# Performance work log

Measured on AMD Instinct MI355X. Metric: run time of the kernel, lower is better.

Reference implementation:

```python
import jax, jax.numpy as jnp
import numpy as np

NUM_USERS = 1000000
NUM_ITEMS = 500000
NUM_R = 5
D = 64
B = 512
N = 30


def _mlp3(x, W1, b1, W2, b2, W3, b3):
    # Linear->ReLU->Linear->ReLU->Linear (as in MLP module)
    h = jax.nn.relu(x @ W1 + b1)
    h = jax.nn.relu(h @ W2 + b2)
    return h @ W3 + b3


def _attn(self_rep, neighs, W1, b1, W2, b2):
    # pi_rep = self_rep.unsqueeze(1).expand_as(neighs)
    rep = jnp.broadcast_to(jnp.expand_dims(self_rep, 1), neighs.shape)
    h = jax.nn.relu(jnp.concatenate([rep, neighs], -1) @ W1 + b1)
    s = h @ W2 + b2
    # NOTE: original torch code uses F.softmax(..., dim=0) (over the batch axis); kept faithfully
    return jax.nn.softmax(s, axis=0)


def _forward(fl, nodes_u, nodes_i, u_items_list, u_users_list, i_users_list,
             u_items_r, u_users_items, u_users_items_r, i_users_r):
    (E_u, E_i, E_r,
     gv_W1, gv_b1, gv_W2, gv_b2, gv_W3, gv_b3,
     attI_W1, attI_b1, attI_W2, attI_b2,
     attO_W1, attO_b1, attO_W2, attO_b2,
     attS_W1, attS_b1, attS_W2, attS_b2,
     atti_W1, atti_b1, atti_W2, atti_b2,
     linI_W, linI_b, linO_W, linO_b,
     umlp_W1, umlp_b1, umlp_W2, umlp_b2, umlp_W3, umlp_b3,
     gu_W1, gu_b1, gu_W2, gu_b2, gu_W3, gu_b3,
     ilin_W, ilin_b,
     g_W1, g_b1, g_W2, g_b2, g_W3, g_b3) = fl

    # ----- UserModeling: item-space aggregation -----
    pi = E_u[nodes_u]                                   # [B, d]
    er = E_r[u_items_r]                                 # [B, N, d]
    qa = E_i[u_items_list]                              # [B, N, d]
    xia = _mlp3(jnp.concatenate([qa, er], -1), gv_W1, gv_b1, gv_W2, gv_b2, gv_W3, gv_b3)
    alpha_ia = _attn(pi, xia, attI_W1, attI_b1, attI_W2, attI_b2)   # [B, N, 1]
    hi_I = jax.nn.relu(jnp.sum(alpha_ia * xia, 1) @ linI_W + linI_b)  # [B, d]

    # ----- UserModeling: social-space aggregation -----
    po = E_u[u_users_list]                              # [B, N, d]
    ero = E_r[u_users_items_r]                          # [B, N, N, d]
    qao = E_i[u_users_items]                            # [B, N, N, d]
    xoa = _mlp3(jnp.concatenate([qao, ero], -1), gv_W1, gv_b1, gv_W2, gv_b2, gv_W3, gv_b3)
    alpha_oa = _attn(po, xoa, attO_W1, attO_b1, attO_W2, attO_b2)   # [B, N, N, 1]
    ho_I = jax.nn.relu(jnp.sum(alpha_oa * xoa, 1) @ linO_W + linO_b)  # [B, N, d]
    # original att_S(ho_I, pi) does not shape-check; intended semantics: pi is self, ho_I are neighbors
    beta_io = _attn(pi, ho_I, attS_W1, attS_b1, attS_W2, attS_b2)   # [B, N, 1]
    hi_S = jax.nn.relu(jnp.sum(beta_io * ho_I, 1) @ linO_W + linO_b)  # original reuses linO (linS unused)
    hi = _mlp3(jnp.concatenate([hi_I, hi_S], -1), umlp_W1, umlp_b1, umlp_W2, umlp_b2, umlp_W3, umlp_b3)

    # ----- ItemModeling -----
    qj = E_i[nodes_i]                                   # [B, d]
    pt = E_u[i_users_list]                              # [B, N, d]
    er2 = E_r[i_users_r]                                # [B, N, d]
    fjt = _mlp3(jnp.concatenate([pt, er2], -1), gu_W1, gu_b1, gu_W2, gu_b2, gu_W3, gu_b3)
    mu_jt = _attn(qj, fjt, atti_W1, atti_b1, atti_W2, atti_b2)      # [B, N, 1]
    zj = jax.nn.relu(jnp.sum(mu_jt * fjt, 1) @ ilin_W + ilin_b)     # [B, d]

    # ----- Rating prediction -----
    gl = _mlp3(jnp.concatenate([hi, zj], -1), g_W1, g_b1, g_W2, g_b2, g_W3, g_b3)  # [B, 1]
    return gl


def setup_inputs() -> dict:
    key = jax.random.key(0)
    ks = iter(jax.random.split(key, 80))
    def P(*shape):
        return jax.random.normal(next(ks), shape, jnp.float32) * 0.05
    def I(shape, hi):
        return jax.random.randint(next(ks), shape, 0, hi, dtype=jnp.int32)
    d = D
    inp = {}
    inp['E_u'] = P(NUM_USERS, d)
    inp['E_i'] = P(NUM_ITEMS, d)
    inp['E_r'] = P(NUM_R, d)
    for pre in ['gv', 'umlp', 'gu']:
        inp[pre + '_W1'] = P(2 * d, d); inp[pre + '_b1'] = P(d)
        inp[pre + '_W2'] = P(d, d);     inp[pre + '_b2'] = P(d)
        inp[pre + '_W3'] = P(d, d);     inp[pre + '_b3'] = P(d)
    for pre in ['attI', 'attO', 'attS', 'atti']:
        inp[pre + '_W1'] = P(2 * d, d); inp[pre + '_b1'] = P(d)
        inp[pre + '_W2'] = P(d, 1);     inp[pre + '_b2'] = P(1)
    inp['linI_W'] = P(d, d); inp['linI_b'] = P(d)
    inp['linO_W'] = P(d, d); inp['linO_b'] = P(d)
    inp['ilin_W'] = P(d, d); inp['ilin_b'] = P(d)
    inp['g_W1'] = P(2 * d, 1); inp['g_b1'] = P(1)
    inp['g_W2'] = P(1, 1);     inp['g_b2'] = P(1)
    inp['g_W3'] = P(1, 1);     inp['g_b3'] = P(1)
    inp['nodes_u'] = I((B,), NUM_USERS)
    inp['nodes_i'] = I((B,), NUM_ITEMS)
    inp['u_items_list'] = I((B, N), NUM_ITEMS)
    inp['u_users_list'] = I((B, N), NUM_USERS)
    inp['i_users_list'] = I((B, N), NUM_USERS)
    inp['u_items_r'] = I((B, N), NUM_R)
    inp['u_users_items'] = I((B, N, N), NUM_ITEMS)
    inp['u_users_items_r'] = I((B, N, N), NUM_R)
    inp['i_users_r'] = I((B, N), NUM_R)
    return inp


def reference(E_u, E_i, E_r,
              gv_W1, gv_b1, gv_W2, gv_b2, gv_W3, gv_b3,
              attI_W1, attI_b1, attI_W2, attI_b2,
              attO_W1, attO_b1, attO_W2, attO_b2,
              attS_W1, attS_b1, attS_W2, attS_b2,
              atti_W1, atti_b1, atti_W2, atti_b2,
              linI_W, linI_b, linO_W, linO_b,
              umlp_W1, umlp_b1, umlp_W2, umlp_b2, umlp_W3, umlp_b3,
              gu_W1, gu_b1, gu_W2, gu_b2, gu_W3, gu_b3,
              ilin_W, ilin_b,
              g_W1, g_b1, g_W2, g_b2, g_W3, g_b3,
              nodes_u, nodes_i, u_items_list, u_users_list, i_users_list,
              u_items_r, u_users_items, u_users_items_r, i_users_r):
    fl = (E_u, E_i, E_r,
          gv_W1, gv_b1, gv_W2, gv_b2, gv_W3, gv_b3,
          attI_W1, attI_b1, attI_W2, attI_b2,
          attO_W1, attO_b1, attO_W2, attO_b2,
          attS_W1, attS_b1, attS_W2, attS_b2,
          atti_W1, atti_b1, atti_W2, atti_b2,
          linI_W, linI_b, linO_W, linO_b,
          umlp_W1, umlp_b1, umlp_W2, umlp_b2, umlp_W3, umlp_b3,
          gu_W1, gu_b1, gu_W2, gu_b2, gu_W3, gu_b3,
          ilin_W, ilin_b,
          g_W1, g_b1, g_W2, g_b2, g_W3, g_b3)
    return _forward(fl, nodes_u, nodes_i, u_items_list, u_users_list, i_users_list,
                    u_items_r, u_users_items, u_users_items_r, i_users_r)
```

## Files before the change

### kernel.cpp

```cpp
#include <hip/hip_runtime.h>
#include <cstdint>
#include <cstddef>


#define GB 512
#define GN 30
#define GD 64

typedef unsigned short u16;
typedef __attribute__((ext_vector_type(8))) short short8v;
typedef __attribute__((ext_vector_type(4))) float f32x4;

__device__ __forceinline__ u16 f2bf(float x) {
  union { float f; uint32_t u; } c; c.f = x;
  uint32_t r = c.u + 0x7fffu + ((c.u >> 16) & 1u);
  return (u16)(r >> 16);
}
__device__ __forceinline__ float bf2f(u16 b) {
  union { float f; uint32_t u; } c; c.u = ((uint32_t)b) << 16; return c.f;
}
__device__ __forceinline__ float wave_sum(float v) {
#pragma unroll
  for (int off = 32; off >= 1; off >>= 1) v += __shfl_xor(v, off, 64);
  return v;
}


__device__ __forceinline__ void mfma_3layers(
    int lane, int wave,
    const u16* xs, const u16* w1s, const u16* w2s, const u16* w3s,
    const float* b1s, const float* b2s, u16* hs, f32x4* c3) {
  const int m = lane & 15, quad = lane >> 4;
  const int row = wave * 16 + m;
  const f32x4 zz = {0.f, 0.f, 0.f, 0.f};
  f32x4 cc[4];
#pragma unroll
  for (int c = 0; c < 4; c++) cc[c] = zz;
#pragma unroll
  for (int kk = 0; kk < 4; kk++) {
    short8v av = *(const short8v*)(xs + row * 136 + kk * 32 + quad * 8);
#pragma unroll
    for (int c = 0; c < 4; c++) {
      short8v bv = *(const short8v*)(w1s + (c * 16 + m) * 136 + kk * 32 + quad * 8);
      cc[c] = __builtin_amdgcn_mfma_f32_16x16x32_bf16(av, bv, cc[c], 0, 0, 0);
    }
  }
#pragma unroll
  for (int c = 0; c < 4; c++)
#pragma unroll
    for (int r = 0; r < 4; r++) {
      int rr = wave * 16 + quad * 4 + r;
      hs[rr * 72 + c * 16 + m] = f2bf(fmaxf(cc[c][r] + b1s[c * 16 + m], 0.f));
    }
#pragma unroll
  for (int c = 0; c < 4; c++) cc[c] = zz;
#pragma unroll
  for (int kk = 0; kk < 2; kk++) {
    short8v av = *(const short8v*)(hs + row * 72 + kk * 32 + quad * 8);
#pragma unroll
    for (int c = 0; c < 4; c++) {
      short8v bv = *(const short8v*)(w2s + (c * 16 + m) * 72 + kk * 32 + quad * 8);
      cc[c] = __builtin_amdgcn_mfma_f32_16x16x32_bf16(av, bv, cc[c], 0, 0, 0);
    }
  }
#pragma unroll
  for (int c = 0; c < 4; c++)
#pragma unroll
    for (int r = 0; r < 4; r++) {
      int rr = wave * 16 + quad * 4 + r;
      hs[rr * 72 + c * 16 + m] = f2bf(fmaxf(cc[c][r] + b2s[c * 16 + m], 0.f));
    }
#pragma unroll
  for (int c = 0; c < 4; c++) c3[c] = zz;
#pragma unroll
  for (int kk = 0; kk < 2; kk++) {
    short8v av = *(const short8v*)(hs + row * 72 + kk * 32 + quad * 8);
#pragma unroll
    for (int c = 0; c < 4; c++) {
      short8v bv = *(const short8v*)(w3s + (c * 16 + m) * 72 + kk * 32 + quad * 8);
      c3[c] = __builtin_amdgcn_mfma_f32_16x16x32_bf16(av, bv, c3[c], 0, 0, 0);
    }
  }
}

__global__ void k_prep(const float* __restrict__ gvW1, const float* __restrict__ gvW2,
                       const float* __restrict__ gvW3, const float* __restrict__ aOW1,
                       const float* __restrict__ guW1, const float* __restrict__ guW2,
                       const float* __restrict__ guW3,
                       u16* gv1t, u16* gv2t, u16* gv3t, u16* aot,
                       u16* gu1t, u16* gu2t, u16* gu3t) {
  int i = blockIdx.x * 256 + threadIdx.x;
  const float* src; u16* dst; int sh; int o = i;
  if (o < 8192)        { src = gvW1;           dst = gv1t; sh = 7; }
  else if (o < 12288)  { o -= 8192;  src = gvW2; dst = gv2t; sh = 6; }
  else if (o < 16384)  { o -= 12288; src = gvW3; dst = gv3t; sh = 6; }
  else if (o < 20480)  { o -= 16384; src = aOW1 + 64 * 64; dst = aot; sh = 6; }
  else if (o < 28672)  { o -= 20480; src = guW1; dst = gu1t; sh = 7; }
  else if (o < 32768)  { o -= 28672; src = guW2; dst = gu2t; sh = 6; }
  else                 { o -= 32768; src = guW3; dst = gu3t; sh = 6; }
  int n = o >> sh, k = o & ((1 << sh) - 1);
  dst[(size_t)n * (1 << sh) + k] = f2bf(src[(size_t)k * 64 + n]);
}

__global__ __launch_bounds__(256, 2) void k_mlp3_mfma(
    const float* __restrict__ tabA, const int* __restrict__ idxA,
    const float* __restrict__ tabB, const int* __restrict__ idxB,
    const u16* __restrict__ w1t, const u16* __restrict__ w2t, const u16* __restrict__ w3t,
    const float* __restrict__ b1, const float* __restrict__ b2, const float* __restrict__ b3,
    float* __restrict__ out) {
  __shared__ __align__(16) u16 xs[64 * 136], w1s[64 * 136], w2s[64 * 72], w3s[64 * 72], hs[64 * 72];
  __shared__ float b1s[64], b2s[64], b3s[64];
  int t = threadIdx.x;
  for (int i = t; i < 64 * 16; i += 256) { int n = i >> 4, j = i & 15;
    ((uint4*)(w1s + n * 136))[j] = ((const uint4*)(w1t + n * 128))[j]; }
  for (int i = t; i < 64 * 8; i += 256) { int n = i >> 3, j = i & 7;
    ((uint4*)(w2s + n * 72))[j] = ((const uint4*)(w2t + n * 64))[j];
    ((uint4*)(w3s + n * 72))[j] = ((const uint4*)(w3t + n * 64))[j]; }
  if (t < 64) { b1s[t] = b1[t]; b2s[t] = b2[t]; b3s[t] = b3[t]; }
  int base = blockIdx.x * 64;
  { int lr = t >> 2, q = t & 3; int row = base + lr;
    const float* src = (q < 2) ? (tabA + (size_t)idxA[row] * 64 + q * 32)
                               : (tabB + (size_t)idxB[row] * 64 + (q - 2) * 32);
    u16* dst = xs + lr * 136 + q * 32;
    const float4* s4 = (const float4*)src;
#pragma unroll
    for (int h = 0; h < 8; h++) { float4 v = s4[h]; ushort4 u;
      u.x = f2bf(v.x); u.y = f2bf(v.y); u.z = f2bf(v.z); u.w = f2bf(v.w);
      *(ushort4*)(dst + h * 4) = u; }
  }
  __syncthreads();
  int lane = t & 63, wave = t >> 6;
  f32x4 c3[4];
  mfma_3layers(lane, wave, xs, w1s, w2s, w3s, b1s, b2s, hs, c3);
  int m = lane & 15, quad = lane >> 4;
#pragma unroll
  for (int c = 0; c < 4; c++)
#pragma unroll
    for (int r = 0; r < 4; r++) {
      int rr = wave * 16 + quad * 4 + r;
      out[(size_t)(base + rr) * 64 + c * 16 + m] = c3[c][r] + b3s[c * 16 + m];
    }
}

__global__ __launch_bounds__(256, 2) void k_xoa1_mfma(
    const float* __restrict__ E_i, const float* __restrict__ E_r,
    const int* __restrict__ items, const int* __restrict__ items_r,
    const u16* __restrict__ w1t, const u16* __restrict__ w2t, const u16* __restrict__ w3t,
    const float* __restrict__ b1, const float* __restrict__ b2, const float* __restrict__ b3,
    const u16* __restrict__ aot, const float* __restrict__ ab1,
    const float* __restrict__ aW2, const float* __restrict__ ab2,
    const float* __restrict__ poW, u16* __restrict__ xoa_bf,
    float* __restrict__ sOut) {
  __shared__ __align__(16) u16 xs[64 * 136], w1s[64 * 136], w2s[64 * 72], w3s[64 * 72], was[64 * 72], hs[64 * 72];
  __shared__ float b1s[64], b2s[64], b3s[64], ab1s[64], aw2s[64];
  int t = threadIdx.x;
  for (int i = t; i < 64 * 16; i += 256) { int n = i >> 4, j = i & 15;
    ((uint4*)(w1s + n * 136))[j] = ((const uint4*)(w1t + n * 128))[j]; }
  for (int i = t; i < 64 * 8; i += 256) { int n = i >> 3, j = i & 7;
    ((uint4*)(w2s + n * 72))[j] = ((const uint4*)(w2t + n * 64))[j];
    ((uint4*)(w3s + n * 72))[j] = ((const uint4*)(w3t + n * 64))[j];
    ((uint4*)(was + n * 72))[j] = ((const uint4*)(aot + n * 64))[j]; }
  if (t < 64) { b1s[t] = b1[t]; b2s[t] = b2[t]; b3s[t] = b3[t];
                ab1s[t] = ab1[t]; aw2s[t] = aW2[t]; }
  __syncthreads();
  const int lane = t & 63, wave = t >> 6;
  const int m = lane & 15, quad = lane >> 4;
  const int lr = t >> 2, q = t & 3;
  const float ab2v = ab2[0];
  const f32x4 zz = {0.f, 0.f, 0.f, 0.f};
  for (int tile = blockIdx.x; tile < (GB * GN * GN) / 64; tile += gridDim.x) {
    int base = tile * 64;
    { int row = base + lr;
      const float* src = (q < 2) ? (E_i + (size_t)items[row] * 64 + q * 32)
                                 : (E_r + (size_t)items_r[row] * 64 + (q - 2) * 32);
      u16* dst = xs + lr * 136 + q * 32;
      const float4* s4 = (const float4*)src;
#pragma unroll
      for (int h = 0; h < 8; h++) { float4 v = s4[h]; ushort4 u;
        u.x = f2bf(v.x); u.y = f2bf(v.y); u.z = f2bf(v.z); u.w = f2bf(v.w);
        *(ushort4*)(dst + h * 4) = u; }
    }
    f32x4 c3[4];
    mfma_3layers(lane, wave, xs, w1s, w2s, w3s, b1s, b2s, hs, c3);
#pragma unroll
    for (int c = 0; c < 4; c++)
#pragma unroll
      for (int r = 0; r < 4; r++) {
        int rr = wave * 16 + quad * 4 + r;
        hs[rr * 72 + c * 16 + m] = f2bf(c3[c][r] + b3s[c * 16 + m]);
      }
#pragma unroll
    for (int c2 = 0; c2 < 2; c2++) {
      int chunk = lane * 2 + c2;
      int row = chunk >> 3, k = chunk & 7;
      *(uint4*)(xoa_bf + ((size_t)(base + wave * 16 + row)) * 64 + k * 8) =
          *(const uint4*)(hs + (wave * 16 + row) * 72 + k * 8);
    }
    f32x4 c4[4];
#pragma unroll
    for (int c = 0; c < 4; c++) c4[c] = zz;
    int row = wave * 16 + m;
#pragma unroll
    for (int kk = 0; kk < 2; kk++) {
      short8v av = *(const short8v*)(hs + row * 72 + kk * 32 + quad * 8);
#pragma unroll
      for (int c = 0; c < 4; c++) {
        short8v bv = *(const short8v*)(was + (c * 16 + m) * 72 + kk * 32 + quad * 8);
        c4[c] = __builtin_amdgcn_mfma_f32_16x16x32_bf16(av, bv, c4[c], 0, 0, 0);
      }
    }
    float part[4] = {0.f, 0.f, 0.f, 0.f};
#pragma unroll
    for (int r = 0; r < 4; r++) {
      int gRow = base + wave * 16 + quad * 4 + r;
      int b_ = gRow / (GN * GN);
      int n2 = gRow % GN;
      const float* pw = poW + ((size_t)b_ * GN + n2) * 64;
#pragma unroll
      for (int c = 0; c < 4; c++) {
        int col = c * 16 + m;
        float h = c4[c][r] + pw[col] + ab1s[col];
        part[r] += fmaxf(h, 0.f) * aw2s[col];
      }
    }
#pragma unroll
    for (int r = 0; r < 4; r++) {
      float v = part[r];
      v += __shfl_xor(v, 1, 64); v += __shfl_xor(v, 2, 64);
      v += __shfl_xor(v, 4, 64); v += __shfl_xor(v, 8, 64);
      if (m == 0) sOut[base + wave * 16 + quad * 4 + r] = v + ab2v;
    }
  }
}

__global__ __launch_bounds__(256) void k_ho(
    const u16* __restrict__ xoa_bf, const float* __restrict__ alpha,
    const float* __restrict__ linW, const float* __restrict__ linB,
    float* __restrict__ ho) {
  __shared__ float lws[64 * 64];
  __shared__ float lbs[64];
  __shared__ float ts[4][64];
  int t = threadIdx.x;
  for (int i = t; i < 4096; i += 256) lws[i] = linW[i];
  if (t < 64) lbs[t] = linB[t];
  __syncthreads();
  int lane = t & 63, wave = t >> 6;
  int gid = blockIdx.x * 4 + wave;
  int b_ = gid / GN, n2 = gid - b_ * GN;
  float acc = 0.f;
  for (int n1 = 0; n1 < GN; n1++) {
    size_t row = (size_t)(b_ * GN + n1) * GN + n2;
    float al = alpha[row];
    acc = fmaf(al, bf2f(xoa_bf[row * 64 + lane]), acc);
  }
  ts[wave][lane] = acc;
  float o = lbs[lane];
#pragma unroll 8
  for (int k = 0; k < 64; k++) o = fmaf(ts[wave][k], lws[k * 64 + lane], o);
  ho[(size_t)gid * 64 + lane] = fmaxf(o, 0.f);
}

template <int R>
__device__ __forceinline__ void mlp3_rows(
    int lane, const float* const* pa, const float* const* pb,
    const u16* w1s, const u16* w2s, const u16* w3s,
    const float* b1s, const float* b2s, const float* b3s,
    float (*hbw)[GD], float* acc) {
#pragma unroll
  for (int r = 0; r < R; r++) acc[r] = b1s[lane];
#pragma unroll 8
  for (int k = 0; k < 64; k++) {
    float w = bf2f(w1s[k * 64 + lane]);
#pragma unroll
    for (int r = 0; r < R; r++) acc[r] = fmaf(pa[r][k], w, acc[r]);
  }
#pragma unroll 8
  for (int k = 0; k < 64; k++) {
    float w = bf2f(w1s[(64 + k) * 64 + lane]);
#pragma unroll
    for (int r = 0; r < R; r++) acc[r] = fmaf(pb[r][k], w, acc[r]);
  }
#pragma unroll
  for (int r = 0; r < R; r++) hbw[r][lane] = fmaxf(acc[r], 0.f);
#pragma unroll
  for (int r = 0; r < R; r++) acc[r] = b2s[lane];
#pragma unroll
  for (int kc = 0; kc < 16; kc++) {
    float w0 = bf2f(w2s[(kc * 4 + 0) * 64 + lane]);
    float w1 = bf2f(w2s[(kc * 4 + 1) * 64 + lane]);
    float w2 = bf2f(w2s[(kc * 4 + 2) * 64 + lane]);
    float w3 = bf2f(w2s[(kc * 4 + 3) * 64 + lane]);
#pragma unroll
    for (int r = 0; r < R; r++) {
      float4 x = *(const float4*)(&hbw[r][kc * 4]);
      acc[r] = fmaf(x.x, w0, fmaf(x.y, w1, fmaf(x.z, w2, fmaf(x.w, w3, acc[r]))));
    }
  }
#pragma unroll
  for (int r = 0; r < R; r++) hbw[r][lane] = fmaxf(acc[r], 0.f);
#pragma unroll
  for (int r = 0; r < R; r++) acc[r] = b3s[lane];
#pragma unroll
  for (int kc = 0; kc < 16; kc++) {
    float w0 = bf2f(w3s[(kc * 4 + 0) * 64 + lane]);
    float w1 = bf2f(w3s[(kc * 4 + 1) * 64 + lane]);
    float w2 = bf2f(w3s[(kc * 4 + 2) * 64 + lane]);
    float w3 = bf2f(w3s[(kc * 4 + 3) * 64 + lane]);
#pragma unroll
    for (int r = 0; r < R; r++) {
      float4 x = *(const float4*)(&hbw[r][kc * 4]);
      acc[r] = fmaf(x.x, w0, fmaf(x.y, w1, fmaf(x.z, w2, fmaf(x.w, w3, acc[r]))));
    }
  }
}

__global__ __launch_bounds__(256, 4) void k_rowlin(
    int M, const float* __restrict__ tab, const int* __restrict__ idx,
    const float* __restrict__ W, float* __restrict__ out) {
  __shared__ float ws[64 * 64];
  for (int i = threadIdx.x; i < 64 * 64; i += 256) ws[i] = W[i];
  __syncthreads();
  const int lane = threadIdx.x & 63, wave = threadIdx.x >> 6;
  int base0 = (blockIdx.x * 4 + wave) * 8;
  if (base0 >= M) return;
  const float* p[8];
#pragma unroll
  for (int r = 0; r < 8; r++) {
    int ia = __builtin_amdgcn_readfirstlane(idx[base0 + r]);
    p[r] = tab + (size_t)ia * 64;
  }
  float acc[8];
#pragma unroll
  for (int r = 0; r < 8; r++) acc[r] = 0.f;
#pragma unroll 8
  for (int k = 0; k < 64; k++) {
    float w = ws[k * 64 + lane];
#pragma unroll
    for (int r = 0; r < 8; r++) acc[r] = fmaf(p[r][k], w, acc[r]);
  }
#pragma unroll
  for (int r = 0; r < 8; r++) out[(size_t)(base0 + r) * 64 + lane] = acc[r];
}

__global__ __launch_bounds__(512, 2) void k_mlp3(
    int M,
    const float* __restrict__ tabA, const int* __restrict__ idxA,
    const float* __restrict__ tabB, const int* __restrict__ idxB,
    const float* __restrict__ W1, const float* __restrict__ b1,
    const float* __restrict__ W2, const float* __restrict__ b2,
    const float* __restrict__ W3, const float* __restrict__ b3,
    float* __restrict__ out) {
  __shared__ u16 w1s[128 * 64], w2s[64 * 64], w3s[64 * 64];
  __shared__ float b1s[64], b2s[64], b3s[64];
  __shared__ float hb[8][8][GD];
  for (int i = threadIdx.x; i < 128 * 64; i += 512) w1s[i] = f2bf(W1[i]);
  for (int i = threadIdx.x; i < 64 * 64; i += 512) { w2s[i] = f2bf(W2[i]); w3s[i] = f2bf(W3[i]); }
  if (threadIdx.x < 64) { b1s[threadIdx.x] = b1[threadIdx.x]; b2s[threadIdx.x] = b2[threadIdx.x]; b3s[threadIdx.x] = b3[threadIdx.x]; }
  __syncthreads();
  const int lane = threadIdx.x & 63, wave = threadIdx.x >> 6;
  for (int base = blockIdx.x * 64; base < M; base += gridDim.x * 64) {
    int rb = base + wave * 8;
    const float* pa[8]; const float* pb[8];
#pragma unroll
    for (int r = 0; r < 8; r++) {
      int row = rb + r;
      int ia = idxA ? idxA[row] : row;
      pa[r] = tabA + (size_t)__builtin_amdgcn_readfirstlane(ia) * 64;
      int ib = idxB ? idxB[row] : row;
      pb[r] = tabB + (size_t)__builtin_amdgcn_readfirstlane(ib) * 64;
    }
    float acc[8];
    mlp3_rows<8>(lane, pa, pb, w1s, w2s, w3s, b1s, b2s, b3s, hb[wave], acc);
#pragma unroll
    for (int r = 0; r < 8; r++) out[(size_t)(rb + r) * 64 + lane] = acc[r];
  }
}

__global__ __launch_bounds__(256, 4) void k_score(
    int M, const float* __restrict__ selfW, const float* __restrict__ X,
    const float* __restrict__ W1b, const float* __restrict__ b1,
    const float* __restrict__ W2, const float* __restrict__ b2,
    float* __restrict__ sOut) {
  __shared__ float ws[64 * 64];
  __shared__ float w2s[64], b1s[64];
  for (int i = threadIdx.x; i < 64 * 64; i += 256) ws[i] = W1b[i];
  if (threadIdx.x < 64) { w2s[threadIdx.x] = W2[threadIdx.x]; b1s[threadIdx.x] = b1[threadIdx.x]; }
  __syncthreads();
  const int lane = threadIdx.x & 63, wave = threadIdx.x >> 6;
  int rb = (blockIdx.x * 4 + wave) * 8;
  if (rb >= M) return;
  const float* px[8]; float acc[8];
#pragma unroll
  for (int r = 0; r < 8; r++) {
    int row = rb + r;
    px[r] = X + (size_t)row * 64;
    acc[r] = b1s[lane] + selfW[(size_t)(row / GN) * 64 + lane];
  }
#pragma unroll 8
  for (int k = 0; k < 64; k++) {
    float w = ws[k * 64 + lane];
#pragma unroll
    for (int r = 0; r < 8; r++) acc[r] = fmaf(px[r][k], w, acc[r]);
  }
  float bb2 = b2[0];
#pragma unroll
  for (int r = 0; r < 8; r++) {
    float v = fmaxf(acc[r], 0.f) * w2s[lane];
    v = wave_sum(v);
    if (lane == 0) sOut[rb + r] = v + bb2;
  }
}

__global__ __launch_bounds__(256) void k_softmax_col(float* __restrict__ s, int C) {
  int c = blockIdx.x, t = threadIdx.x;
  int lane = t & 63, wave = t >> 6;
  float v0 = s[(size_t)t * C + c];
  float v1 = s[(size_t)(t + 256) * C + c];
  float m = fmaxf(v0, v1);
#pragma unroll
  for (int off = 32; off >= 1; off >>= 1) m = fmaxf(m, __shfl_xor(m, off, 64));
  __shared__ float rm[4], rs[4];
  if (lane == 0) rm[wave] = m;
  __syncthreads();
  float M4 = fmaxf(fmaxf(rm[0], rm[1]), fmaxf(rm[2], rm[3]));
  float e0 = expf(v0 - M4), e1 = expf(v1 - M4);
  float sm = wave_sum(e0 + e1);
  if (lane == 0) rs[wave] = sm;
  __syncthreads();
  float inv = 1.f / (rs[0] + rs[1] + rs[2] + rs[3]);
  s[(size_t)t * C + c] = e0 * inv;
  s[(size_t)(t + 256) * C + c] = e1 * inv;
}

__global__ __launch_bounds__(64) void k_wsum_lin(
    int C, const float* __restrict__ alpha, const float* __restrict__ X,
    const float* __restrict__ W, const float* __restrict__ bias,
    float* __restrict__ out) {
  int b = blockIdx.x, l = threadIdx.x;
  float t = 0.f;
  for (int n = 0; n < C; n++) t = fmaf(alpha[b * C + n], X[((size_t)b * C + n) * 64 + l], t);
  __shared__ float ts[64];
  ts[l] = t;
  float acc = bias[l];
#pragma unroll 8
  for (int k = 0; k < 64; k++) acc = fmaf(ts[k], W[k * 64 + l], acc);
  out[(size_t)b * 64 + l] = fmaxf(acc, 0.f);
}

__global__ __launch_bounds__(256) void k_final(
    const float* __restrict__ hi, const float* __restrict__ zj,
    const float* __restrict__ gW1, const float* __restrict__ gb1,
    const float* __restrict__ gW2, const float* __restrict__ gb2,
    const float* __restrict__ gW3, const float* __restrict__ gb3,
    float* __restrict__ out) {
  const int lane = threadIdx.x & 63, wave = threadIdx.x >> 6;
  int b = blockIdx.x * 4 + wave;
  float v = hi[(size_t)b * 64 + lane] * gW1[lane] + zj[(size_t)b * 64 + lane] * gW1[64 + lane];
  v = wave_sum(v);
  if (lane == 0) {
    float h = fmaxf(v + gb1[0], 0.f);
    h = fmaxf(h * gW2[0] + gb2[0], 0.f);
    out[b] = h * gW3[0] + gb3[0];
  }
}

extern "C" void kernel_launch(void* const* d_in, const int* in_sizes, int n_in,
                              void* d_out, int out_size, void* d_ws, size_t ws_size,
                              hipStream_t stream) {
  const float* E_u = (const float*)d_in[0];
  const float* E_i = (const float*)d_in[1];
  const float* E_r = (const float*)d_in[2];
  const float* gvW1 = (const float*)d_in[3];  const float* gvb1 = (const float*)d_in[4];
  const float* gvW2 = (const float*)d_in[5];  const float* gvb2 = (const float*)d_in[6];
  const float* gvW3 = (const float*)d_in[7];  const float* gvb3 = (const float*)d_in[8];
  const float* umW1 = (const float*)d_in[9];  const float* umb1 = (const float*)d_in[10];
  const float* umW2 = (const float*)d_in[11]; const float* umb2 = (const float*)d_in[12];
  const float* umW3 = (const float*)d_in[13]; const float* umb3 = (const float*)d_in[14];
  const float* guW1 = (const float*)d_in[15]; const float* gub1 = (const float*)d_in[16];
  const float* guW2 = (const float*)d_in[17]; const float* gub2 = (const float*)d_in[18];
  const float* guW3 = (const float*)d_in[19]; const float* gub3 = (const float*)d_in[20];
  const float* aIW1 = (const float*)d_in[21]; const float* aIb1 = (const float*)d_in[22];
  const float* aIW2 = (const float*)d_in[23]; const float* aIb2 = (const float*)d_in[24];
  const float* aOW1 = (const float*)d_in[25]; const float* aOb1 = (const float*)d_in[26];
  const float* aOW2 = (const float*)d_in[27]; const float* aOb2 = (const float*)d_in[28];
  const float* aSW1 = (const float*)d_in[29]; const float* aSb1 = (const float*)d_in[30];
  const float* aSW2 = (const float*)d_in[31]; const float* aSb2 = (const float*)d_in[32];
  const float* aiW1 = (const float*)d_in[33]; const float* aib1 = (const float*)d_in[34];
  const float* aiW2 = (const float*)d_in[35]; const float* aib2 = (const float*)d_in[36];
  const float* linIW = (const float*)d_in[37]; const float* linIb = (const float*)d_in[38];
  const float* linOW = (const float*)d_in[39]; const float* linOb = (const float*)d_in[40];
  const float* ilinW = (const float*)d_in[41]; const float* ilinb = (const float*)d_in[42];
  const float* gW1 = (const float*)d_in[43]; const float* gb1 = (const float*)d_in[44];
  const float* gW2 = (const float*)d_in[45]; const float* gb2 = (const float*)d_in[46];
  const float* gW3 = (const float*)d_in[47]; const float* gb3 = (const float*)d_in[48];
  const int* nodes_u = (const int*)d_in[49];
  const int* nodes_i = (const int*)d_in[50];
  const int* u_items = (const int*)d_in[51];
  const int* u_users = (const int*)d_in[52];
  const int* i_users = (const int*)d_in[53];
  const int* u_items_r = (const int*)d_in[54];
  const int* uu_items = (const int*)d_in[55];
  const int* uu_items_r = (const int*)d_in[56];
  const int* i_users_r = (const int*)d_in[57];
  float* out = (float*)d_out;

  float* p = (float*)d_ws;
  float* piWI = p; p += GB * GD;
  float* piWS = p; p += GB * GD;
  float* qjWi = p; p += GB * GD;
  float* poW  = p; p += GB * GN * GD;
  float* xia  = p; p += GB * GN * GD;
  float* fjt  = p; p += GB * GN * GD;
  float* ho   = p; p += GB * GN * GD;
  float* sI   = p; p += GB * GN;
  float* sS   = p; p += GB * GN;
  float* si   = p; p += GB * GN;
  float* sO   = p; p += GB * GN * GN;
  float* hiI  = p; p += GB * GD;
  float* hiS  = p; p += GB * GD;
  float* hi   = p; p += GB * GD;
  float* zj   = p; p += GB * GD;
  u16* q16 = (u16*)p;
  u16* gv1t = q16; q16 += 8192;
  u16* gv2t = q16; q16 += 4096;
  u16* gv3t = q16; q16 += 4096;
  u16* aot  = q16; q16 += 4096;
  u16* gu1t = q16; q16 += 8192;
  u16* gu2t = q16; q16 += 4096;
  u16* gu3t = q16; q16 += 4096;
  u16* xoa_bf = q16; q16 += (size_t)GB * GN * GN * GD;

  const int BN = GB * GN;
  const int M2 = GB * GN * GN;

  k_prep<<<144, 256, 0, stream>>>(gvW1, gvW2, gvW3, aOW1, guW1, guW2, guW3,
                                  gv1t, gv2t, gv3t, aot, gu1t, gu2t, gu3t);
  k_rowlin<<<GB / 32, 256, 0, stream>>>(GB, E_u, nodes_u, aIW1, piWI);
  k_rowlin<<<GB / 32, 256, 0, stream>>>(GB, E_u, nodes_u, aSW1, piWS);
  k_rowlin<<<GB / 32, 256, 0, stream>>>(GB, E_i, nodes_i, aiW1, qjWi);
  k_rowlin<<<BN / 32, 256, 0, stream>>>(BN, E_u, u_users, aOW1, poW);

  k_mlp3_mfma<<<BN / 64, 256, 0, stream>>>(E_i, u_items, E_r, u_items_r,
                                           gv1t, gv2t, gv3t, gvb1, gvb2, gvb3, xia);
  k_score<<<BN / 32, 256, 0, stream>>>(BN, piWI, xia, aIW1 + 64 * 64, aIb1, aIW2, aIb2, sI);
  k_softmax_col<<<GN, 256, 0, stream>>>(sI, GN);
  k_wsum_lin<<<GB, 64, 0, stream>>>(GN, sI, xia, linIW, linIb, hiI);

  k_xoa1_mfma<<<512, 256, 0, stream>>>(E_i, E_r, uu_items, uu_items_r,
                                       gv1t, gv2t, gv3t, gvb1, gvb2, gvb3,
                                       aot, aOb1, aOW2, aOb2, poW, xoa_bf, sO);
  k_softmax_col<<<GN * GN, 256, 0, stream>>>(sO, GN * GN);
  k_ho<<<BN / 4, 256, 0, stream>>>(xoa_bf, sO, linOW, linOb, ho);
  k_score<<<BN / 32, 256, 0, stream>>>(BN, piWS, ho, aSW1 + 64 * 64, aSb1, aSW2, aSb2, sS);
  k_softmax_col<<<GN, 256, 0, stream>>>(sS, GN);
  k_wsum_lin<<<GB, 64, 0, stream>>>(GN, sS, ho, linOW, linOb, hiS);
  k_mlp3<<<GB / 64, 512, 0, stream>>>(GB, hiI, nullptr, hiS, nullptr,
                                      umW1, umb1, umW2, umb2, umW3, umb3, hi);

  k_mlp3_mfma<<<BN / 64, 256, 0, stream>>>(E_u, i_users, E_r, i_users_r,
                                           gu1t, gu2t, gu3t, gub1, gub2, gub3, fjt);
  k_score<<<BN / 32, 256, 0, stream>>>(BN, qjWi, fjt, aiW1 + 64 * 64, aib1, aiW2, aib2, si);
  k_softmax_col<<<GN, 256, 0, stream>>>(si, GN);
  k_wsum_lin<<<GB, 64, 0, stream>>>(GN, si, fjt, ilinW, ilinb, zj);

  k_final<<<GB / 4, 256, 0, stream>>>(hi, zj, gW1, gb1, gW2, gb2, gW3, gb3, out);
}
```

Baseline: 722.4 us.

## Merge pipeline into setup, fused MLP-attention engine, aggregation and tail kernels

Replaces about twenty launches with roughly eight. Weight prep and the row projections are merged into one setup kernel. All three MLP+attention-score paths (xoa, xia, fjt) run in one persistent engine kernel that keeps the layer-2, layer-3 and attention weights in registers and prefetches the next tile's gathered rows. The intermediates xia and fjt are now stored as bf16, scores are stored transposed for softmax, and the user MLP plus the final MLP are fused into one MFMA tail kernel. The aim is to cut launch overhead, shared-memory weight traffic and global intermediate bandwidth, at the cost of higher register pressure and some extra bf16 precision loss.

After: 616.5 us. -14.7%, faster.

```diff
diff --git a/kernel.cpp b/kernel.cpp
--- a/kernel.cpp
+++ b/kernel.cpp
@@ -6,6 +6,7 @@
 #define GB 512
 #define GN 30
 #define GD 64
+#define IDX16(l) ((((l) & 15) << 2) | ((l) >> 4))
 
 typedef unsigned short u16;
 typedef __attribute__((ext_vector_type(8))) short short8v;
@@ -25,362 +26,316 @@
   return v;
 }
 
-
-__device__ __forceinline__ void mfma_3layers(
-    int lane, int wave,
-    const u16* xs, const u16* w1s, const u16* w2s, const u16* w3s,
-    const float* b1s, const float* b2s, u16* hs, f32x4* c3) {
-  const int m = lane & 15, quad = lane >> 4;
-  const int row = wave * 16 + m;
-  const f32x4 zz = {0.f, 0.f, 0.f, 0.f};
-  f32x4 cc[4];
-#pragma unroll
-  for (int c = 0; c < 4; c++) cc[c] = zz;
-#pragma unroll
-  for (int kk = 0; kk < 4; kk++) {
-    short8v av = *(const short8v*)(xs + row * 136 + kk * 32 + quad * 8);
-#pragma unroll
-    for (int c = 0; c < 4; c++) {
-      short8v bv = *(const short8v*)(w1s + (c * 16 + m) * 136 + kk * 32 + quad * 8);
-      cc[c] = __builtin_amdgcn_mfma_f32_16x16x32_bf16(av, bv, cc[c], 0, 0, 0);
-    }
-  }
-#pragma unroll
-  for (int c = 0; c < 4; c++)
-#pragma unroll
-    for (int r = 0; r < 4; r++) {
-      int rr = wave * 16 + quad * 4 + r;
-      hs[rr * 72 + c * 16 + m] = f2bf(fmaxf(cc[c][r] + b1s[c * 16 + m], 0.f));
-    }
-#pragma unroll
-  for (int c = 0; c < 4; c++) cc[c] = zz;
-#pragma unroll
-  for (int kk = 0; kk < 2; kk++) {
-    short8v av = *(const short8v*)(hs + row * 72 + kk * 32 + quad * 8);
-#pragma unroll
-    for (int c = 0; c < 4; c++) {
-      short8v bv = *(const short8v*)(w2s + (c * 16 + m) * 72 + kk * 32 + quad * 8);
-      cc[c] = __builtin_amdgcn_mfma_f32_16x16x32_bf16(av, bv, cc[c], 0, 0, 0);
-    }
-  }
-#pragma unroll
-  for (int c = 0; c < 4; c++)
-#pragma unroll
-    for (int r = 0; r < 4; r++) {
-      int rr = wave * 16 + quad * 4 + r;
-      hs[rr * 72 + c * 16 + m] = f2bf(fmaxf(cc[c][r] + b2s[c * 16 + m], 0.f));
-    }
-#pragma unroll
-  for (int c = 0; c < 4; c++) c3[c] = zz;
-#pragma unroll
-  for (int kk = 0; kk < 2; kk++) {
-    short8v av = *(const short8v*)(hs + row * 72 + kk * 32 + quad * 8);
-#pragma unroll
-    for (int c = 0; c < 4; c++) {
-      short8v bv = *(const short8v*)(w3s + (c * 16 + m) * 72 + kk * 32 + quad * 8);
-      c3[c] = __builtin_amdgcn_mfma_f32_16x16x32_bf16(av, bv, c3[c], 0, 0, 0);
-    }
-  }
-}
-
-__global__ void k_prep(const float* __restrict__ gvW1, const float* __restrict__ gvW2,
-                       const float* __restrict__ gvW3, const float* __restrict__ aOW1,
-                       const float* __restrict__ guW1, const float* __restrict__ guW2,
-                       const float* __restrict__ guW3,
-                       u16* gv1t, u16* gv2t, u16* gv3t, u16* aot,
-                       u16* gu1t, u16* gu2t, u16* gu3t) {
-  int i = blockIdx.x * 256 + threadIdx.x;
-  const float* src; u16* dst; int sh; int o = i;
-  if (o < 8192)        { src = gvW1;           dst = gv1t; sh = 7; }
-  else if (o < 12288)  { o -= 8192;  src = gvW2; dst = gv2t; sh = 6; }
-  else if (o < 16384)  { o -= 12288; src = gvW3; dst = gv3t; sh = 6; }
-  else if (o < 20480)  { o -= 16384; src = aOW1 + 64 * 64; dst = aot; sh = 6; }
-  else if (o < 28672)  { o -= 20480; src = guW1; dst = gu1t; sh = 7; }
-  else if (o < 32768)  { o -= 28672; src = guW2; dst = gu2t; sh = 6; }
-  else                 { o -= 32768; src = guW3; dst = gu3t; sh = 6; }
-  int n = o >> sh, k = o & ((1 << sh) - 1);
-  dst[(size_t)n * (1 << sh) + k] = f2bf(src[(size_t)k * 64 + n]);
-}
-
-__global__ __launch_bounds__(256, 2) void k_mlp3_mfma(
-    const float* __restrict__ tabA, const int* __restrict__ idxA,
-    const float* __restrict__ tabB, const int* __restrict__ idxB,
-    const u16* __restrict__ w1t, const u16* __restrict__ w2t, const u16* __restrict__ w3t,
-    const float* __restrict__ b1, const float* __restrict__ b2, const float* __restrict__ b3,
-    float* __restrict__ out) {
-  __shared__ __align__(16) u16 xs[64 * 136], w1s[64 * 136], w2s[64 * 72], w3s[64 * 72], hs[64 * 72];
-  __shared__ float b1s[64], b2s[64], b3s[64];
-  int t = threadIdx.x;
+__global__ __launch_bounds__(256) void k_setup(
+    const float* __restrict__ gvW1, const float* __restrict__ gvW2, const float* __restrict__ gvW3,
+    const float* __restrict__ guW1, const float* __restrict__ guW2, const float* __restrict__ guW3,
+    const float* __restrict__ umW1, const float* __restrict__ umW2, const float* __restrict__ umW3,
+    const float* __restrict__ aOW1, const float* __restrict__ aIW1, const float* __restrict__ aiW1,
+    const float* __restrict__ aSW1,
+    const float* __restrict__ E_u, const float* __restrict__ E_i,
+    const int* __restrict__ nodes_u, const int* __restrict__ nodes_i, const int* __restrict__ u_users,
+    u16* gv1t, u16* gv2t, u16* gv3t, u16* gu1t, u16* gu2t, u16* gu3t,
+    u16* um1t, u16* um2t, u16* um3t, u16* aOt, u16* aIt, u16* ait,
+    float* piWI, float* piWS, float* qjWi, float* poW) {
+  __shared__ float ws[64 * 64];
+  int blk = blockIdx.x, t = threadIdx.x;
+  if (blk < 240) {
+    int o = blk * 256 + t;
+    const float* src; u16* dst; int kind;
+    if      (o < 8192)  {            src = gvW1; dst = gv1t; kind = 0; }
+    else if (o < 12288) { o -= 8192;  src = gvW2; dst = gv2t; kind = 1; }
+    else if (o < 16384) { o -= 12288; src = gvW3; dst = gv3t; kind = 1; }
+    else if (o < 20480) { o -= 16384; src = aOW1; dst = aOt;  kind = 2; }
+    else if (o < 28672) { o -= 20480; src = guW1; dst = gu1t; kind = 0; }
+    else if (o < 32768) { o -= 28672; src = guW2; dst = gu2t; kind = 1; }
+    else if (o < 36864) { o -= 32768; src = guW3; dst = gu3t; kind = 1; }
+    else if (o < 40960) { o -= 36864; src = aIW1; dst = aIt;  kind = 2; }
+    else if (o < 45056) { o -= 40960; src = aiW1; dst = ait;  kind = 2; }
+    else if (o < 53248) { o -= 45056; src = umW1; dst = um1t; kind = 0; }
+    else if (o < 57344) { o -= 53248; src = umW2; dst = um2t; kind = 1; }
+    else                { o -= 57344; src = umW3; dst = um3t; kind = 1; }
+    if (kind == 0) { int n = o >> 7, k = o & 127; dst[n * 128 + k] = f2bf(src[(size_t)k * 64 + n]); }
+    else { int n = o >> 6, p = o & 63; int k = ((p & 3) << 4) | (p >> 2); if (kind == 2) k += 64;
+           dst[n * 64 + p] = f2bf(src[(size_t)k * 64 + n]); }
+    return;
+  }
+  int rb = blk - 240;
+  const float* tab; const int* idx; const float* W; float* out; int base;
+  if (rb < 16)      { tab = E_u; idx = nodes_u; W = aIW1; out = piWI; base = rb * 32; }
+  else if (rb < 32) { tab = E_u; idx = nodes_u; W = aSW1; out = piWS; base = (rb - 16) * 32; }
+  else if (rb < 48) { tab = E_i; idx = nodes_i; W = aiW1; out = qjWi; base = (rb - 32) * 32; }
+  else              { tab = E_u; idx = u_users; W = aOW1; out = poW;  base = (rb - 48) * 32; }
+  for (int i = t; i < 4096; i += 256) ws[i] = W[i];
+  __syncthreads();
+  int lane = t & 63, wave = t >> 6;
+  int b0 = base + wave * 8;
+  const float* p[8]; float acc[8];
+#pragma unroll
+  for (int r = 0; r < 8; r++) {
+    p[r] = tab + (size_t)__builtin_amdgcn_readfirstlane(idx[b0 + r]) * 64;
+    acc[r] = 0.f;
+  }
+#pragma unroll 8
+  for (int k = 0; k < 64; k++) {
+    float w = ws[k * 64 + lane];
+#pragma unroll
+    for (int r = 0; r < 8; r++) acc[r] = fmaf(p[r][k], w, acc[r]);
+  }
+#pragma unroll
+  for (int r = 0; r < 8; r++) out[(size_t)(b0 + r) * 64 + lane] = acc[r];
+}
+
+__global__ __launch_bounds__(256, 2) void k_engine(
+    const float* __restrict__ E_i, const float* __restrict__ E_r, const float* __restrict__ E_u,
+    const int* __restrict__ uu_items, const int* __restrict__ uu_items_r,
+    const int* __restrict__ u_items, const int* __restrict__ u_items_r,
+    const int* __restrict__ i_users, const int* __restrict__ i_users_r,
+    const u16* __restrict__ gv1t, const u16* __restrict__ gv2t, const u16* __restrict__ gv3t,
+    const u16* __restrict__ gu1t, const u16* __restrict__ gu2t, const u16* __restrict__ gu3t,
+    const float* __restrict__ gvb1, const float* __restrict__ gvb2, const float* __restrict__ gvb3,
+    const float* __restrict__ gub1, const float* __restrict__ gub2, const float* __restrict__ gub3,
+    const u16* __restrict__ aOt, const u16* __restrict__ aIt, const u16* __restrict__ ait,
+    const float* __restrict__ aOb1, const float* __restrict__ aIb1, const float* __restrict__ aib1,
+    const float* __restrict__ aOW2, const float* __restrict__ aIW2, const float* __restrict__ aiW2,
+    const float* __restrict__ aOb2, const float* __restrict__ aIb2, const float* __restrict__ aib2,
+    const float* __restrict__ poW, const float* __restrict__ piWI, const float* __restrict__ qjWi,
+    u16* __restrict__ xoa_bf, u16* __restrict__ xia_bf, u16* __restrict__ fjt_bf,
+    float* __restrict__ sOT, float* __restrict__ sIT, float* __restrict__ siT) {
+  __shared__ __align__(16) u16 xs[64 * 136], w1s[64 * 136], hs[64 * 72];
+  __shared__ float b1s[64], b2s[64], b3s[64], ab1s[64], aw2s[64];
+  int t = threadIdx.x, blk = blockIdx.x;
+  const float *tabA, *tabB, *selfW, *b1, *b2, *b3, *ab1, *aW2, *ab2p;
+  const int *idxA, *idxB; const u16 *w1t, *w2t, *w3t, *att;
+  u16* outB; float* sT; int tile0, modeNN;
+  if (blk < 480) {
+    tabA = E_i; idxA = uu_items; tabB = E_r; idxB = uu_items_r;
+    w1t = gv1t; w2t = gv2t; w3t = gv3t; b1 = gvb1; b2 = gvb2; b3 = gvb3;
+    att = aOt; ab1 = aOb1; aW2 = aOW2; ab2p = aOb2; selfW = poW;
+    outB = xoa_bf; sT = sOT; tile0 = blk * 15; modeNN = 1;
+  } else if (blk < 496) {
+    int lb = blk - 480;
+    tabA = E_i; idxA = u_items; tabB = E_r; idxB = u_items_r;
+    w1t = gv1t; w2t = gv2t; w3t = gv3t; b1 = gvb1; b2 = gvb2; b3 = gvb3;
+    att = aIt; ab1 = aIb1; aW2 = aIW2; ab2p = aIb2; selfW = piWI;
+    outB = xia_bf; sT = sIT; tile0 = lb * 15; modeNN = 0;
+  } else {
+    int lb = blk - 496;
+    tabA = E_u; idxA = i_users; tabB = E_r; idxB = i_users_r;
+    w1t = gu1t; w2t = gu2t; w3t = gu3t; b1 = gub1; b2 = gub2; b3 = gub3;
+    att = ait; ab1 = aib1; aW2 = aiW2; ab2p = aib2; selfW = qjWi;
+    outB = fjt_bf; sT = siT; tile0 = lb * 15; modeNN = 0;
+  }
+  const int nt = 15;
   for (int i = t; i < 64 * 16; i += 256) { int n = i >> 4, j = i & 15;
     ((uint4*)(w1s + n * 136))[j] = ((const uint4*)(w1t + n * 128))[j]; }
-  for (int i = t; i < 64 * 8; i += 256) { int n = i >> 3, j = i & 7;
-    ((uint4*)(w2s + n * 72))[j] = ((const uint4*)(w2t + n * 64))[j];
-    ((uint4*)(w3s + n * 72))[j] = ((const uint4*)(w3t + n * 64))[j]; }
-  if (t < 64) { b1s[t] = b1[t]; b2s[t] = b2[t]; b3s[t] = b3[t]; }
-  int base = blockIdx.x * 64;
-  { int lr = t >> 2, q = t & 3; int row = base + lr;
+  if (t < 64) { b1s[t] = b1[t]; b2s[t] = b2[t]; b3s[t] = b3[t];
+                ab1s[t] = ab1[t]; aw2s[t] = aW2[t]; }
+  __syncthreads();
+  const int lane = t & 63, wave = t >> 6, m = lane & 15, quad = lane >> 4;
+  const int lr = t >> 2, q = t & 3;
+  short8v w2f[8], w3f[8], waf[8];
+#pragma unroll
+  for (int c = 0; c < 4; c++)
+#pragma unroll
+    for (int kk = 0; kk < 2; kk++) {
+      int off = (c * 16 + m) * 64 + kk * 32 + quad * 8;
+      w2f[c * 2 + kk] = *(const short8v*)(w2t + off);
+      w3f[c * 2 + kk] = *(const short8v*)(w3t + off);
+      waf[c * 2 + kk] = *(const short8v*)(att + off);
+    }
+  const float ab2v = ab2p[0];
+  const f32x4 zz = {0.f, 0.f, 0.f, 0.f};
+  float4 fr[8];
+  {
+    int row = tile0 * 64 + lr;
     const float* src = (q < 2) ? (tabA + (size_t)idxA[row] * 64 + q * 32)
                                : (tabB + (size_t)idxB[row] * 64 + (q - 2) * 32);
-    u16* dst = xs + lr * 136 + q * 32;
-    const float4* s4 = (const float4*)src;
-#pragma unroll
-    for (int h = 0; h < 8; h++) { float4 v = s4[h]; ushort4 u;
-      u.x = f2bf(v.x); u.y = f2bf(v.y); u.z = f2bf(v.z); u.w = f2bf(v.w);
-      *(ushort4*)(dst + h * 4) = u; }
-  }
-  __syncthreads();
-  int lane = t & 63, wave = t >> 6;
-  f32x4 c3[4];
-  mfma_3layers(lane, wave, xs, w1s, w2s, w3s, b1s, b2s, hs, c3);
-  int m = lane & 15, quad = lane >> 4;
-#pragma unroll
-  for (int c = 0; c < 4; c++)
-#pragma unroll
-    for (int r = 0; r < 4; r++) {
-      int rr = wave * 16 + quad * 4 + r;
-      out[(size_t)(base + rr) * 64 + c * 16 + m] = c3[c][r] + b3s[c * 16 + m];
-    }
-}
-
-__global__ __launch_bounds__(256, 2) void k_xoa1_mfma(
-    const float* __restrict__ E_i, const float* __restrict__ E_r,
-    const int* __restrict__ items, const int* __restrict__ items_r,
-    const u16* __restrict__ w1t, const u16* __restrict__ w2t, const u16* __restrict__ w3t,
-    const float* __restrict__ b1, const float* __restrict__ b2, const float* __restrict__ b3,
-    const u16* __restrict__ aot, const float* __restrict__ ab1,
-    const float* __restrict__ aW2, const float* __restrict__ ab2,
-    const float* __restrict__ poW, u16* __restrict__ xoa_bf,
-    float* __restrict__ sOut) {
-  __shared__ __align__(16) u16 xs[64 * 136], w1s[64 * 136], w2s[64 * 72], w3s[64 * 72], was[64 * 72], hs[64 * 72];
-  __shared__ float b1s[64], b2s[64], b3s[64], ab1s[64], aw2s[64];
-  int t = threadIdx.x;
-  for (int i = t; i < 64 * 16; i += 256) { int n = i >> 4, j = i & 15;
-    ((uint4*)(w1s + n * 136))[j] = ((const uint4*)(w1t + n * 128))[j]; }
-  for (int i = t; i < 64 * 8; i += 256) { int n = i >> 3, j = i & 7;
-    ((uint4*)(w2s + n * 72))[j] = ((const uint4*)(w2t + n * 64))[j];
-    ((uint4*)(w3s + n * 72))[j] = ((const uint4*)(w3t + n * 64))[j];
-    ((uint4*)(was + n * 72))[j] = ((const uint4*)(aot + n * 64))[j]; }
-  if (t < 64) { b1s[t] = b1[t]; b2s[t] = b2[t]; b3s[t] = b3[t];
-                ab1s[t] = ab1[t]; aw2s[t] = aW2[t]; }
-  __syncthreads();
-  const int lane = t & 63, wave = t >> 6;
-  const int m = lane & 15, quad = lane >> 4;
-  const int lr = t >> 2, q = t & 3;
-  const float ab2v = ab2[0];
-  const f32x4 zz = {0.f, 0.f, 0.f, 0.f};
-  for (int tile = blockIdx.x; tile < (GB * GN * GN) / 64; tile += gridDim.x) {
-    int base = tile * 64;
-    { int row = base + lr;
-      const float* src = (q < 2) ? (E_i + (size_t)items[row] * 64 + q * 32)
-                                 : (E_r + (size_t)items_r[row] * 64 + (q - 2) * 32);
-      u16* dst = xs + lr * 136 + q * 32;
-      const float4* s4 = (const float4*)src;
-#pragma unroll
-      for (int h = 0; h < 8; h++) { float4 v = s4[h]; ushort4 u;
+#pragma unroll
+    for (int h = 0; h < 8; h++) fr[h] = ((const float4*)src)[h];
+  }
+  for (int it = 0; it < nt; it++) {
+    int base = (tile0 + it) * 64;
+    { u16* dst = xs + lr * 136 + q * 32;
+#pragma unroll
+      for (int h = 0; h < 8; h++) { float4 v = fr[h]; ushort4 u;
         u.x = f2bf(v.x); u.y = f2bf(v.y); u.z = f2bf(v.z); u.w = f2bf(v.w);
-        *(ushort4*)(dst + h * 4) = u; }
-    }
+        *(ushort4*)(dst + h * 4) = u; } }
+    if (it + 1 < nt) {
+      int row = base + 64 + lr;
+      const float* src = (q < 2) ? (tabA + (size_t)idxA[row] * 64 + q * 32)
+                                 : (tabB + (size_t)idxB[row] * 64 + (q - 2) * 32);
+#pragma unroll
+      for (int h = 0; h < 8; h++) fr[h] = ((const float4*)src)[h];
+    }
+    f32x4 cc[4];
+#pragma unroll
+    for (int c = 0; c < 4; c++) cc[c] = zz;
+#pragma unroll
+    for (int kk = 0; kk < 4; kk++) {
+      short8v av = *(const short8v*)(xs + (wave * 16 + m) * 136 + kk * 32 + quad * 8);
+#pragma unroll
+      for (int c = 0; c < 4; c++) {
+        short8v bv = *(const short8v*)(w1s + (c * 16 + m) * 136 + kk * 32 + quad * 8);
+        cc[c] = __builtin_amdgcn_mfma_f32_16x16x32_bf16(av, bv, cc[c], 0, 0, 0);
+      }
+    }
+#pragma unroll
+    for (int r = 0; r < 4; r++) { ushort4 u;
+      u.x = f2bf(fmaxf(cc[0][r] + b1s[m], 0.f));
+      u.y = f2bf(fmaxf(cc[1][r] + b1s[16 + m], 0.f));
+      u.z = f2bf(fmaxf(cc[2][r] + b1s[32 + m], 0.f));
+      u.w = f2bf(fmaxf(cc[3][r] + b1s[48 + m], 0.f));
+      *(ushort4*)(hs + (wave * 16 + quad * 4 + r) * 72 + m * 4) = u; }
+#pragma unroll
+    for (int c = 0; c < 4; c++) cc[c] = zz;
+#pragma unroll
+    for (int kk = 0; kk < 2; kk++) {
+      short8v av = *(const short8v*)(hs + (wave * 16 + m) * 72 + kk * 32 + quad * 8);
+#pragma unroll
+      for (int c = 0; c < 4; c++)
+        cc[c] = __builtin_amdgcn_mfma_f32_16x16x32_bf16(av, w2f[c * 2 + kk], cc[c], 0, 0, 0);
+    }
+#pragma unroll
+    for (int r = 0; r < 4; r++) { ushort4 u;
+      u.x = f2bf(fmaxf(cc[0][r] + b2s[m], 0.f));
+      u.y = f2bf(fmaxf(cc[1][r] + b2s[16 + m], 0.f));
+      u.z = f2bf(fmaxf(cc[2][r] + b2s[32 + m], 0.f));
+      u.w = f2bf(fmaxf(cc[3][r] + b2s[48 + m], 0.f));
+      *(ushort4*)(hs + (wave * 16 + quad * 4 + r) * 72 + m * 4) = u; }
     f32x4 c3[4];
-    mfma_3layers(lane, wave, xs, w1s, w2s, w3s, b1s, b2s, hs, c3);
-#pragma unroll
-    for (int c = 0; c < 4; c++)
-#pragma unroll
-      for (int r = 0; r < 4; r++) {
-        int rr = wave * 16 + quad * 4 + r;
-        hs[rr * 72 + c * 16 + m] = f2bf(c3[c][r] + b3s[c * 16 + m]);
-      }
+#pragma unroll
+    for (int c = 0; c < 4; c++) c3[c] = zz;
+#pragma unroll
+    for (int kk = 0; kk < 2; kk++) {
+      short8v av = *(const short8v*)(hs + (wave * 16 + m) * 72 + kk * 32 + quad * 8);
+#pragma unroll
+      for (int c = 0; c < 4; c++)
+        c3[c] = __builtin_amdgcn_mfma_f32_16x16x32_bf16(av, w3f[c * 2 + kk], c3[c], 0, 0, 0);
+    }
+#pragma unroll
+    for (int r = 0; r < 4; r++) { ushort4 u;
+      u.x = f2bf(c3[0][r] + b3s[m]);
+      u.y = f2bf(c3[1][r] + b3s[16 + m]);
+      u.z = f2bf(c3[2][r] + b3s[32 + m]);
+      u.w = f2bf(c3[3][r] + b3s[48 + m]);
+      *(ushort4*)(hs + (wave * 16 + quad * 4 + r) * 72 + m * 4) = u; }
 #pragma unroll
     for (int c2 = 0; c2 < 2; c2++) {
-      int chunk = lane * 2 + c2;
-      int row = chunk >> 3, k = chunk & 7;
-      *(uint4*)(xoa_bf + ((size_t)(base + wave * 16 + row)) * 64 + k * 8) =
-          *(const uint4*)(hs + (wave * 16 + row) * 72 + k * 8);
+      int chunk = lane * 2 + c2; int row = chunk >> 3, k8 = chunk & 7;
+      *(uint4*)(outB + ((size_t)(base + wave * 16 + row)) * 64 + k8 * 8) =
+          *(const uint4*)(hs + (wave * 16 + row) * 72 + k8 * 8);
     }
     f32x4 c4[4];
 #pragma unroll
     for (int c = 0; c < 4; c++) c4[c] = zz;
-    int row = wave * 16 + m;
 #pragma unroll
     for (int kk = 0; kk < 2; kk++) {
-      short8v av = *(const short8v*)(hs + row * 72 + kk * 32 + quad * 8);
-#pragma unroll
-      for (int c = 0; c < 4; c++) {
-        short8v bv = *(const short8v*)(was + (c * 16 + m) * 72 + kk * 32 + quad * 8);
-        c4[c] = __builtin_amdgcn_mfma_f32_16x16x32_bf16(av, bv, c4[c], 0, 0, 0);
-      }
-    }
-    float part[4] = {0.f, 0.f, 0.f, 0.f};
+      short8v av = *(const short8v*)(hs + (wave * 16 + m) * 72 + kk * 32 + quad * 8);
+#pragma unroll
+      for (int c = 0; c < 4; c++)
+        c4[c] = __builtin_amdgcn_mfma_f32_16x16x32_bf16(av, waf[c * 2 + kk], c4[c], 0, 0, 0);
+    }
+    float part[4];
 #pragma unroll
     for (int r = 0; r < 4; r++) {
       int gRow = base + wave * 16 + quad * 4 + r;
-      int b_ = gRow / (GN * GN);
-      int n2 = gRow % GN;
-      const float* pw = poW + ((size_t)b_ * GN + n2) * 64;
+      int sidx = modeNN ? ((gRow / (GN * GN)) * GN + gRow % GN) : (gRow / GN);
+      const float* pw = selfW + (size_t)sidx * 64;
+      float s = 0.f;
 #pragma unroll
       for (int c = 0; c < 4; c++) {
         int col = c * 16 + m;
-        float h = c4[c][r] + pw[col] + ab1s[col];
-        part[r] += fmaxf(h, 0.f) * aw2s[col];
+        s += fmaxf(c4[c][r] + pw[col] + ab1s[col], 0.f) * aw2s[col];
       }
+      part[r] = s;
     }
 #pragma unroll
     for (int r = 0; r < 4; r++) {
       float v = part[r];
       v += __shfl_xor(v, 1, 64); v += __shfl_xor(v, 2, 64);
       v += __shfl_xor(v, 4, 64); v += __shfl_xor(v, 8, 64);
-      if (m == 0) sOut[base + wave * 16 + quad * 4 + r] = v + ab2v;
-    }
-  }
-}
-
-__global__ __launch_bounds__(256) void k_ho(
-    const u16* __restrict__ xoa_bf, const float* __restrict__ alpha,
-    const float* __restrict__ linW, const float* __restrict__ linB,
-    float* __restrict__ ho) {
-  __shared__ float lws[64 * 64];
-  __shared__ float lbs[64];
+      if (m == 0) {
+        int gRow = base + wave * 16 + quad * 4 + r;
+        int scol, sb;
+        if (modeNN) { sb = gRow / (GN * GN); scol = gRow % (GN * GN); }
+        else        { sb = gRow / GN;        scol = gRow % GN; }
+        sT[(size_t)scol * GB + sb] = v + ab2v;
+      }
+    }
+  }
+}
+
+__global__ __launch_bounds__(256) void k_softmax_t(
+    float* __restrict__ sIT, float* __restrict__ siT, float* __restrict__ sOT) {
+  int blk = blockIdx.x, t = threadIdx.x;
+  float* p;
+  if (blk < 30)      p = sIT + (size_t)blk * GB;
+  else if (blk < 60) p = siT + (size_t)(blk - 30) * GB;
+  else               p = sOT + (size_t)(blk - 60) * GB;
+  int lane = t & 63, wave = t >> 6;
+  float v0 = p[t], v1 = p[t + 256];
+  float mx = fmaxf(v0, v1);
+#pragma unroll
+  for (int off = 32; off >= 1; off >>= 1) mx = fmaxf(mx, __shfl_xor(mx, off, 64));
+  __shared__ float rm[4], rs[4];
+  if (lane == 0) rm[wave] = mx;
+  __syncthreads();
+  float M4 = fmaxf(fmaxf(rm[0], rm[1]), fmaxf(rm[2], rm[3]));
+  float e0 = expf(v0 - M4), e1 = expf(v1 - M4);
+  float sm = wave_sum(e0 + e1);
+  if (lane == 0) rs[wave] = sm;
+  __syncthreads();
+  float inv = 1.f / (rs[0] + rs[1] + rs[2] + rs[3]);
+  p[t] = e0 * inv;
+  p[t + 256] = e1 * inv;
+}
+
+__global__ __launch_bounds__(256) void k_agg(
+    const u16* __restrict__ xia_bf, const u16* __restrict__ fjt_bf, const u16* __restrict__ xoa_bf,
+    const float* __restrict__ sIT, const float* __restrict__ siT, const float* __restrict__ sOT,
+    const float* __restrict__ linIW, const float* __restrict__ linIb,
+    const float* __restrict__ ilinW, const float* __restrict__ ilinb,
+    const float* __restrict__ linOW, const float* __restrict__ linOb,
+    float* __restrict__ hiI, float* __restrict__ zj, float* __restrict__ ho) {
+  __shared__ float ws[64 * 64];
   __shared__ float ts[4][64];
-  int t = threadIdx.x;
-  for (int i = t; i < 4096; i += 256) lws[i] = linW[i];
-  if (t < 64) lbs[t] = linB[t];
-  __syncthreads();
-  int lane = t & 63, wave = t >> 6;
-  int gid = blockIdx.x * 4 + wave;
-  int b_ = gid / GN, n2 = gid - b_ * GN;
+  int blk = blockIdx.x, t = threadIdx.x, lane = t & 63, wave = t >> 6;
+  const float* W; const float* bias;
+  if (blk < 128)      { W = linIW; bias = linIb; }
+  else if (blk < 256) { W = ilinW; bias = ilinb; }
+  else                { W = linOW; bias = linOb; }
+  for (int i = t; i < 4096; i += 256) ws[i] = W[i];
+  __syncthreads();
+  int px = IDX16(lane);
   float acc = 0.f;
-  for (int n1 = 0; n1 < GN; n1++) {
-    size_t row = (size_t)(b_ * GN + n1) * GN + n2;
-    float al = alpha[row];
-    acc = fmaf(al, bf2f(xoa_bf[row * 64 + lane]), acc);
+  float* outp;
+  if (blk < 256) {
+    int b = (blk & 127) * 4 + wave;
+    const u16* X = (blk < 128) ? xia_bf : fjt_bf;
+    const float* al = (blk < 128) ? sIT : siT;
+    for (int n = 0; n < GN; n++)
+      acc = fmaf(al[(size_t)n * GB + b], bf2f(X[((size_t)b * GN + n) * 64 + px]), acc);
+    outp = ((blk < 128) ? hiI : zj) + (size_t)b * 64;
+  } else {
+    int gid = (blk - 256) * 4 + wave;
+    int b_ = gid / GN, n2 = gid - b_ * GN;
+    for (int n1 = 0; n1 < GN; n1++)
+      acc = fmaf(sOT[((size_t)(n1 * GN + n2)) * GB + b_],
+                 bf2f(xoa_bf[(((size_t)b_ * GN + n1) * GN + n2) * 64 + px]), acc);
+    outp = ho + (size_t)gid * 64;
   }
   ts[wave][lane] = acc;
-  float o = lbs[lane];
+  float o = bias[lane];
 #pragma unroll 8
-  for (int k = 0; k < 64; k++) o = fmaf(ts[wave][k], lws[k * 64 + lane], o);
-  ho[(size_t)gid * 64 + lane] = fmaxf(o, 0.f);
-}
-
-template <int R>
-__device__ __forceinline__ void mlp3_rows(
-    int lane, const float* const* pa, const float* const* pb,
-    const u16* w1s, const u16* w2s, const u16* w3s,
-    const float* b1s, const float* b2s, const float* b3s,
-    float (*hbw)[GD], float* acc) {
-#pragma unroll
-  for (int r = 0; r < R; r++) acc[r] = b1s[lane];
-#pragma unroll 8
-  for (int k = 0; k < 64; k++) {
-    float w = bf2f(w1s[k * 64 + lane]);
-#pragma unroll
-    for (int r = 0; r < R; r++) acc[r] = fmaf(pa[r][k], w, acc[r]);
-  }
-#pragma unroll 8
-  for (int k = 0; k < 64; k++) {
-    float w = bf2f(w1s[(64 + k) * 64 + lane]);
-#pragma unroll
-    for (int r = 0; r < R; r++) acc[r] = fmaf(pb[r][k], w, acc[r]);
-  }
-#pragma unroll
-  for (int r = 0; r < R; r++) hbw[r][lane] = fmaxf(acc[r], 0.f);
-#pragma unroll
-  for (int r = 0; r < R; r++) acc[r] = b2s[lane];
-#pragma unroll
-  for (int kc = 0; kc < 16; kc++) {
-    float w0 = bf2f(w2s[(kc * 4 + 0) * 64 + lane]);
-    float w1 = bf2f(w2s[(kc * 4 + 1) * 64 + lane]);
-    float w2 = bf2f(w2s[(kc * 4 + 2) * 64 + lane]);
-    float w3 = bf2f(w2s[(kc * 4 + 3) * 64 + lane]);
-#pragma unroll
-    for (int r = 0; r < R; r++) {
-      float4 x = *(const float4*)(&hbw[r][kc * 4]);
-      acc[r] = fmaf(x.x, w0, fmaf(x.y, w1, fmaf(x.z, w2, fmaf(x.w, w3, acc[r]))));
-    }
-  }
-#pragma unroll
-  for (int r = 0; r < R; r++) hbw[r][lane] = fmaxf(acc[r], 0.f);
-#pragma unroll
-  for (int r = 0; r < R; r++) acc[r] = b3s[lane];
-#pragma unroll
-  for (int kc = 0; kc < 16; kc++) {
-    float w0 = bf2f(w3s[(kc * 4 + 0) * 64 + lane]);
-    float w1 = bf2f(w3s[(kc * 4 + 1) * 64 + lane]);
-    float w2 = bf2f(w3s[(kc * 4 + 2) * 64 + lane]);
-    float w3 = bf2f(w3s[(kc * 4 + 3) * 64 + lane]);
-#pragma unroll
-    for (int r = 0; r < R; r++) {
-      float4 x = *(const float4*)(&hbw[r][kc * 4]);
-      acc[r] = fmaf(x.x, w0, fmaf(x.y, w1, fmaf(x.z, w2, fmaf(x.w, w3, acc[r]))));
-    }
-  }
-}
-
-__global__ __launch_bounds__(256, 4) void k_rowlin(
-    int M, const float* __restrict__ tab, const int* __restrict__ idx,
-    const float* __restrict__ W, float* __restrict__ out) {
-  __shared__ float ws[64 * 64];
-  for (int i = threadIdx.x; i < 64 * 64; i += 256) ws[i] = W[i];
-  __syncthreads();
-  const int lane = threadIdx.x & 63, wave = threadIdx.x >> 6;
-  int base0 = (blockIdx.x * 4 + wave) * 8;
-  if (base0 >= M) return;
-  const float* p[8];
-#pragma unroll
-  for (int r = 0; r < 8; r++) {
-    int ia = __builtin_amdgcn_readfirstlane(idx[base0 + r]);
-    p[r] = tab + (size_t)ia * 64;
-  }
-  float acc[8];
-#pragma unroll
-  for (int r = 0; r < 8; r++) acc[r] = 0.f;
-#pragma unroll 8
-  for (int k = 0; k < 64; k++) {
-    float w = ws[k * 64 + lane];
-#pragma unroll
-    for (int r = 0; r < 8; r++) acc[r] = fmaf(p[r][k], w, acc[r]);
-  }
-#pragma unroll
-  for (int r = 0; r < 8; r++) out[(size_t)(base0 + r) * 64 + lane] = acc[r];
-}
-
-__global__ __launch_bounds__(512, 2) void k_mlp3(
-    int M,
-    const float* __restrict__ tabA, const int* __restrict__ idxA,
-    const float* __restrict__ tabB, const int* __restrict__ idxB,
-    const float* __restrict__ W1, const float* __restrict__ b1,
-    const float* __restrict__ W2, const float* __restrict__ b2,
-    const float* __restrict__ W3, const float* __restrict__ b3,
-    float* __restrict__ out) {
-  __shared__ u16 w1s[128 * 64], w2s[64 * 64], w3s[64 * 64];
-  __shared__ float b1s[64], b2s[64], b3s[64];
-  __shared__ float hb[8][8][GD];
-  for (int i = threadIdx.x; i < 128 * 64; i += 512) w1s[i] = f2bf(W1[i]);
-  for (int i = threadIdx.x; i < 64 * 64; i += 512) { w2s[i] = f2bf(W2[i]); w3s[i] = f2bf(W3[i]); }
-  if (threadIdx.x < 64) { b1s[threadIdx.x] = b1[threadIdx.x]; b2s[threadIdx.x] = b2[threadIdx.x]; b3s[threadIdx.x] = b3[threadIdx.x]; }
-  __syncthreads();
-  const int lane = threadIdx.x & 63, wave = threadIdx.x >> 6;
-  for (int base = blockIdx.x * 64; base < M; base += gridDim.x * 64) {
-    int rb = base + wave * 8;
-    const float* pa[8]; const float* pb[8];
-#pragma unroll
-    for (int r = 0; r < 8; r++) {
-      int row = rb + r;
-      int ia = idxA ? idxA[row] : row;
-      pa[r] = tabA + (size_t)__builtin_amdgcn_readfirstlane(ia) * 64;
-      int ib = idxB ? idxB[row] : row;
-      pb[r] = tabB + (size_t)__builtin_amdgcn_readfirstlane(ib) * 64;
-    }
-    float acc[8];
-    mlp3_rows<8>(lane, pa, pb, w1s, w2s, w3s, b1s, b2s, b3s, hb[wave], acc);
-#pragma unroll
-    for (int r = 0; r < 8; r++) out[(size_t)(rb + r) * 64 + lane] = acc[r];
-  }
-}
-
-__global__ __launch_bounds__(256, 4) void k_score(
-    int M, const float* __restrict__ selfW, const float* __restrict__ X,
+  for (int k = 0; k < 64; k++) o = fmaf(ts[wave][k], ws[k * 64 + lane], o);
+  outp[lane] = fmaxf(o, 0.f);
+}
+
+__global__ __launch_bounds__(256, 4) void k_score_sS(
+    const float* __restrict__ selfW, const float* __restrict__ X,
     const float* __restrict__ W1b, const float* __restrict__ b1,
     const float* __restrict__ W2, const float* __restrict__ b2,
-    float* __restrict__ sOut) {
+    float* __restrict__ sT) {
   __shared__ float ws[64 * 64];
   __shared__ float w2s[64], b1s[64];
   for (int i = threadIdx.x; i < 64 * 64; i += 256) ws[i] = W1b[i];
@@ -388,7 +343,6 @@
   __syncthreads();
   const int lane = threadIdx.x & 63, wave = threadIdx.x >> 6;
   int rb = (blockIdx.x * 4 + wave) * 8;
-  if (rb >= M) return;
   const float* px[8]; float acc[8];
 #pragma unroll
   for (int r = 0; r < 8; r++) {
@@ -407,60 +361,130 @@
   for (int r = 0; r < 8; r++) {
     float v = fmaxf(acc[r], 0.f) * w2s[lane];
     v = wave_sum(v);
-    if (lane == 0) sOut[rb + r] = v + bb2;
-  }
-}
-
-__global__ __launch_bounds__(256) void k_softmax_col(float* __restrict__ s, int C) {
-  int c = blockIdx.x, t = threadIdx.x;
-  int lane = t & 63, wave = t >> 6;
-  float v0 = s[(size_t)t * C + c];
-  float v1 = s[(size_t)(t + 256) * C + c];
-  float m = fmaxf(v0, v1);
-#pragma unroll
-  for (int off = 32; off >= 1; off >>= 1) m = fmaxf(m, __shfl_xor(m, off, 64));
-  __shared__ float rm[4], rs[4];
-  if (lane == 0) rm[wave] = m;
-  __syncthreads();
-  float M4 = fmaxf(fmaxf(rm[0], rm[1]), fmaxf(rm[2], rm[3]));
-  float e0 = expf(v0 - M4), e1 = expf(v1 - M4);
-  float sm = wave_sum(e0 + e1);
-  if (lane == 0) rs[wave] = sm;
-  __syncthreads();
-  float inv = 1.f / (rs[0] + rs[1] + rs[2] + rs[3]);
-  s[(size_t)t * C + c] = e0 * inv;
-  s[(size_t)(t + 256) * C + c] = e1 * inv;
-}
-
-__global__ __launch_bounds__(64) void k_wsum_lin(
-    int C, const float* __restrict__ alpha, const float* __restrict__ X,
-    const float* __restrict__ W, const float* __restrict__ bias,
-    float* __restrict__ out) {
-  int b = blockIdx.x, l = threadIdx.x;
-  float t = 0.f;
-  for (int n = 0; n < C; n++) t = fmaf(alpha[b * C + n], X[((size_t)b * C + n) * 64 + l], t);
-  __shared__ float ts[64];
-  ts[l] = t;
-  float acc = bias[l];
+    int row = rb + r;
+    if (lane == 0) sT[(size_t)(row % GN) * GB + row / GN] = v + bb2;
+  }
+}
+
+__global__ __launch_bounds__(256) void k_wsum_hiS(
+    const float* __restrict__ ho, const float* __restrict__ sST,
+    const float* __restrict__ linOW, const float* __restrict__ linOb,
+    float* __restrict__ hiS) {
+  __shared__ float ws[64 * 64];
+  __shared__ float ts[4][64];
+  int t = threadIdx.x, lane = t & 63, wave = t >> 6;
+  for (int i = t; i < 4096; i += 256) ws[i] = linOW[i];
+  __syncthreads();
+  int b = blockIdx.x * 4 + wave;
+  float acc = 0.f;
+  for (int n = 0; n < GN; n++)
+    acc = fmaf(sST[(size_t)n * GB + b], ho[((size_t)b * GN + n) * 64 + lane], acc);
+  ts[wave][lane] = acc;
+  float o = linOb[lane];
 #pragma unroll 8
-  for (int k = 0; k < 64; k++) acc = fmaf(ts[k], W[k * 64 + l], acc);
-  out[(size_t)b * 64 + l] = fmaxf(acc, 0.f);
-}
-
-__global__ __launch_bounds__(256) void k_final(
-    const float* __restrict__ hi, const float* __restrict__ zj,
+  for (int k = 0; k < 64; k++) o = fmaf(ts[wave][k], ws[k * 64 + lane], o);
+  hiS[(size_t)b * 64 + lane] = fmaxf(o, 0.f);
+}
+
+__global__ __launch_bounds__(256, 2) void k_tail(
+    const float* __restrict__ hiI, const float* __restrict__ hiS, const float* __restrict__ zj,
+    const u16* __restrict__ um1t, const u16* __restrict__ um2t, const u16* __restrict__ um3t,
+    const float* __restrict__ umb1, const float* __restrict__ umb2, const float* __restrict__ umb3,
     const float* __restrict__ gW1, const float* __restrict__ gb1,
     const float* __restrict__ gW2, const float* __restrict__ gb2,
     const float* __restrict__ gW3, const float* __restrict__ gb3,
     float* __restrict__ out) {
-  const int lane = threadIdx.x & 63, wave = threadIdx.x >> 6;
-  int b = blockIdx.x * 4 + wave;
-  float v = hi[(size_t)b * 64 + lane] * gW1[lane] + zj[(size_t)b * 64 + lane] * gW1[64 + lane];
-  v = wave_sum(v);
-  if (lane == 0) {
-    float h = fmaxf(v + gb1[0], 0.f);
-    h = fmaxf(h * gW2[0] + gb2[0], 0.f);
-    out[b] = h * gW3[0] + gb3[0];
+  __shared__ __align__(16) u16 xs[64 * 136], w1s[64 * 136], hs[64 * 72];
+  __shared__ float b1s[64], b2s[64], b3s[64], g1s[128];
+  int t = threadIdx.x;
+  for (int i = t; i < 64 * 16; i += 256) { int n = i >> 4, j = i & 15;
+    ((uint4*)(w1s + n * 136))[j] = ((const uint4*)(um1t + n * 128))[j]; }
+  if (t < 64) { b1s[t] = umb1[t]; b2s[t] = umb2[t]; b3s[t] = umb3[t]; }
+  if (t < 128) g1s[t] = gW1[t];
+  int base = blockIdx.x * 64;
+  { int lr = t >> 2, q = t & 3; int b = base + lr;
+    const float* src = (q < 2) ? (hiI + (size_t)b * 64 + q * 32)
+                               : (hiS + (size_t)b * 64 + (q - 2) * 32);
+    u16* dst = xs + lr * 136 + q * 32;
+#pragma unroll
+    for (int h = 0; h < 8; h++) { float4 v = ((const float4*)src)[h]; ushort4 u;
+      u.x = f2bf(v.x); u.y = f2bf(v.y); u.z = f2bf(v.z); u.w = f2bf(v.w);
+      *(ushort4*)(dst + h * 4) = u; } }
+  __syncthreads();
+  const int lane = t & 63, wave = t >> 6, m = lane & 15, quad = lane >> 4;
+  short8v w2f[8], w3f[8];
+#pragma unroll
+  for (int c = 0; c < 4; c++)
+#pragma unroll
+    for (int kk = 0; kk < 2; kk++) {
+      int off = (c * 16 + m) * 64 + kk * 32 + quad * 8;
+      w2f[c * 2 + kk] = *(const short8v*)(um2t + off);
+      w3f[c * 2 + kk] = *(const short8v*)(um3t + off);
+    }
+  const f32x4 zz = {0.f, 0.f, 0.f, 0.f};
+  f32x4 cc[4];
+#pragma unroll
+  for (int c = 0; c < 4; c++) cc[c] = zz;
+#pragma unroll
+  for (int kk = 0; kk < 4; kk++) {
+    short8v av = *(const short8v*)(xs + (wave * 16 + m) * 136 + kk * 32 + quad * 8);
+#pragma unroll
+    for (int c = 0; c < 4; c++) {
+      short8v bv = *(const short8v*)(w1s + (c * 16 + m) * 136 + kk * 32 + quad * 8);
+      cc[c] = __builtin_amdgcn_mfma_f32_16x16x32_bf16(av, bv, cc[c], 0, 0, 0);
+    }
+  }
+#pragma unroll
+  for (int r = 0; r < 4; r++) { ushort4 u;
+    u.x = f2bf(fmaxf(cc[0][r] + b1s[m], 0.f));
+    u.y = f2bf(fmaxf(cc[1][r] + b1s[16 + m], 0.f));
+    u.z = f2bf(fmaxf(cc[2][r] + b1s[32 + m], 0.f));
+    u.w = f2bf(fmaxf(cc[3][r] + b1s[48 + m], 0.f));
+    *(ushort4*)(hs + (wave * 16 + quad * 4 + r) * 72 + m * 4) = u; }
+#pragma unroll
+  for (int c = 0; c < 4; c++) cc[c] = zz;
+#pragma unroll
+  for (int kk = 0; kk < 2; kk++) {
+    short8v av = *(const short8v*)(hs + (wave * 16 + m) * 72 + kk * 32 + quad * 8);
+#pragma unroll
+    for (int c = 0; c < 4; c++)
+      cc[c] = __builtin_amdgcn_mfma_f32_16x16x32_bf16(av, w2f[c * 2 + kk], cc[c], 0, 0, 0);
+  }
+#pragma unroll
+  for (int r = 0; r < 4; r++) { ushort4 u;
+    u.x = f2bf(fmaxf(cc[0][r] + b2s[m], 0.f));
+    u.y = f2bf(fmaxf(cc[1][r] + b2s[16 + m], 0.f));
+    u.z = f2bf(fmaxf(cc[2][r] + b2s[32 + m], 0.f));
+    u.w = f2bf(fmaxf(cc[3][r] + b2s[48 + m], 0.f));
+    *(ushort4*)(hs + (wave * 16 + quad * 4 + r) * 72 + m * 4) = u; }
+  f32x4 c3[4];
+#pragma unroll
+  for (int c = 0; c < 4; c++) c3[c] = zz;
+#pragma unroll
+  for (int kk = 0; kk < 2; kk++) {
+    short8v av = *(const short8v*)(hs + (wave * 16 + m) * 72 + kk * 32 + quad * 8);
+#pragma unroll
+    for (int c = 0; c < 4; c++)
+      c3[c] = __builtin_amdgcn_mfma_f32_16x16x32_bf16(av, w3f[c * 2 + kk], c3[c], 0, 0, 0);
+  }
+#pragma unroll
+  for (int r = 0; r < 4; r++) { ushort4 u;
+    u.x = f2bf(c3[0][r] + b3s[m]);
+    u.y = f2bf(c3[1][r] + b3s[16 + m]);
+    u.z = f2bf(c3[2][r] + b3s[32 + m]);
+    u.w = f2bf(c3[3][r] + b3s[48 + m]);
+    *(ushort4*)(hs + (wave * 16 + quad * 4 + r) * 72 + m * 4) = u; }
+  float gb1v = gb1[0], gb2v = gb2[0], gb3v = gb3[0], gW2v = gW2[0], gW3v = gW3[0];
+  int px = IDX16(lane);
+  for (int r16 = 0; r16 < 16; r16++) {
+    int row = wave * 16 + r16, b = base + row;
+    float v = bf2f(hs[row * 72 + px]) * g1s[lane] + zj[(size_t)b * 64 + lane] * g1s[64 + lane];
+    v = wave_sum(v);
+    if (lane == 0) {
+      float h = fmaxf(v + gb1v, 0.f);
+      h = fmaxf(h * gW2v + gb2v, 0.f);
+      out[b] = h * gW3v + gb3v;
+    }
   }
 }
 
@@ -504,64 +528,62 @@
   const int* i_users_r = (const int*)d_in[57];
   float* out = (float*)d_out;
 
+  const int BN = GB * GN;
+  const int M2 = GB * GN * GN;
+
   float* p = (float*)d_ws;
   float* piWI = p; p += GB * GD;
   float* piWS = p; p += GB * GD;
   float* qjWi = p; p += GB * GD;
-  float* poW  = p; p += GB * GN * GD;
-  float* xia  = p; p += GB * GN * GD;
-  float* fjt  = p; p += GB * GN * GD;
-  float* ho   = p; p += GB * GN * GD;
-  float* sI   = p; p += GB * GN;
-  float* sS   = p; p += GB * GN;
-  float* si   = p; p += GB * GN;
-  float* sO   = p; p += GB * GN * GN;
+  float* poW  = p; p += BN * GD;
+  float* ho   = p; p += BN * GD;
+  float* sIT  = p; p += BN;
+  float* siT  = p; p += BN;
+  float* sST  = p; p += BN;
+  float* sOT  = p; p += M2;
   float* hiI  = p; p += GB * GD;
   float* hiS  = p; p += GB * GD;
-  float* hi   = p; p += GB * GD;
   float* zj   = p; p += GB * GD;
   u16* q16 = (u16*)p;
   u16* gv1t = q16; q16 += 8192;
   u16* gv2t = q16; q16 += 4096;
   u16* gv3t = q16; q16 += 4096;
-  u16* aot  = q16; q16 += 4096;
   u16* gu1t = q16; q16 += 8192;
   u16* gu2t = q16; q16 += 4096;
   u16* gu3t = q16; q16 += 4096;
-  u16* xoa_bf = q16; q16 += (size_t)GB * GN * GN * GD;
-
-  const int BN = GB * GN;
-  const int M2 = GB * GN * GN;
-
-  k_prep<<<144, 256, 0, stream>>>(gvW1, gvW2, gvW3, aOW1, guW1, guW2, guW3,
-                                  gv1t, gv2t, gv3t, aot, gu1t, gu2t, gu3t);
-  k_rowlin<<<GB / 32, 256, 0, stream>>>(GB, E_u, nodes_u, aIW1, piWI);
-  k_rowlin<<<GB / 32, 256, 0, stream>>>(GB, E_u, nodes_u, aSW1, piWS);
-  k_rowlin<<<GB / 32, 256, 0, stream>>>(GB, E_i, nodes_i, aiW1, qjWi);
-  k_rowlin<<<BN / 32, 256, 0, stream>>>(BN, E_u, u_users, aOW1, poW);
-
-  k_mlp3_mfma<<<BN / 64, 256, 0, stream>>>(E_i, u_items, E_r, u_items_r,
-                                           gv1t, gv2t, gv3t, gvb1, gvb2, gvb3, xia);
-  k_score<<<BN / 32, 256, 0, stream>>>(BN, piWI, xia, aIW1 + 64 * 64, aIb1, aIW2, aIb2, sI);
-  k_softmax_col<<<GN, 256, 0, stream>>>(sI, GN);
-  k_wsum_lin<<<GB, 64, 0, stream>>>(GN, sI, xia, linIW, linIb, hiI);
-
-  k_xoa1_mfma<<<512, 256, 0, stream>>>(E_i, E_r, uu_items, uu_items_r,
-                                       gv1t, gv2t, gv3t, gvb1, gvb2, gvb3,
-                                       aot, aOb1, aOW2, aOb2, poW, xoa_bf, sO);
-  k_softmax_col<<<GN * GN, 256, 0, stream>>>(sO, GN * GN);
-  k_ho<<<BN / 4, 256, 0, stream>>>(xoa_bf, sO, linOW, linOb, ho);
-  k_score<<<BN / 32, 256, 0, stream>>>(BN, piWS, ho, aSW1 + 64 * 64, aSb1, aSW2, aSb2, sS);
-  k_softmax_col<<<GN, 256, 0, stream>>>(sS, GN);
-  k_wsum_lin<<<GB, 64, 0, stream>>>(GN, sS, ho, linOW, linOb, hiS);
-  k_mlp3<<<GB / 64, 512, 0, stream>>>(GB, hiI, nullptr, hiS, nullptr,
-                                      umW1, umb1, umW2, umb2, umW3, umb3, hi);
-
-  k_mlp3_mfma<<<BN / 64, 256, 0, stream>>>(E_u, i_users, E_r, i_users_r,
-                                           gu1t, gu2t, gu3t, gub1, gub2, gub3, fjt);
-  k_score<<<BN / 32, 256, 0, stream>>>(BN, qjWi, fjt, aiW1 + 64 * 64, aib1, aiW2, aib2, si);
-  k_softmax_col<<<GN, 256, 0, stream>>>(si, GN);
-  k_wsum_lin<<<GB, 64, 0, stream>>>(GN, si, fjt, ilinW, ilinb, zj);
-
-  k_final<<<GB / 4, 256, 0, stream>>>(hi, zj, gW1, gb1, gW2, gb2, gW3, gb3, out);
-}
+  u16* um1t = q16; q16 += 8192;
+  u16* um2t = q16; q16 += 4096;
+  u16* um3t = q16; q16 += 4096;
+  u16* aOt  = q16; q16 += 4096;
+  u16* aIt  = q16; q16 += 4096;
+  u16* ait  = q16; q16 += 4096;
+  u16* xia_bf = q16; q16 += (size_t)BN * GD;
+  u16* fjt_bf = q16; q16 += (size_t)BN * GD;
+  u16* xoa_bf = q16; q16 += (size_t)M2 * GD;
+
+  k_setup<<<768, 256, 0, stream>>>(gvW1, gvW2, gvW3, guW1, guW2, guW3,
+                                   umW1, umW2, umW3, aOW1, aIW1, aiW1, aSW1,
+                                   E_u, E_i, nodes_u, nodes_i, u_users,
+                                   gv1t, gv2t, gv3t, gu1t, gu2t, gu3t,
+                                   um1t, um2t, um3t, aOt, aIt, ait,
+                                   piWI, piWS, qjWi, poW);
+  k_engine<<<512, 256, 0, stream>>>(E_i, E_r, E_u,
+                                    uu_items, uu_items_r, u_items, u_items_r,
+                                    i_users, i_users_r,
+                                    gv1t, gv2t, gv3t, gu1t, gu2t, gu3t,
+                                    gvb1, gvb2, gvb3, gub1, gub2, gub3,
+                                    aOt, aIt, ait, aOb1, aIb1, aib1,
+                                    aOW2, aIW2, aiW2, aOb2, aIb2, aib2,
+                                    poW, piWI, qjWi,
+                                    xoa_bf, xia_bf, fjt_bf, sOT, sIT, siT);
+  k_softmax_t<<<960, 256, 0, stream>>>(sIT, siT, sOT);
+  k_agg<<<256 + BN / 4, 256, 0, stream>>>(xia_bf, fjt_bf, xoa_bf, sIT, siT, sOT,
+                                          linIW, linIb, ilinW, ilinb, linOW, linOb,
+                                          hiI, zj, ho);
+  k_score_sS<<<BN / 32, 256, 0, stream>>>(piWS, ho, aSW1 + 64 * 64, aSb1, aSW2, aSb2, sST);
+  k_softmax_t<<<30, 256, 0, stream>>>(sST, sST, sST);
+  k_wsum_hiS<<<GB / 4, 256, 0, stream>>>(ho, sST, linOW, linOb, hiS);
+  k_tail<<<GB / 64, 256, 0, stream>>>(hiI, hiS, zj, um1t, um2t, um3t,
+                                      umb1, umb2, umb3,
+                                      gW1, gb1, gW2, gb2, gW3, gb3, out);
+}
```
